# Kernel optimization log

Measured on AMD Instinct MI355X. Metric: run time of the kernel, lower is better.

Reference implementation:

```python
import jax, jax.numpy as jnp
import numpy as np

N = 100000       # nodes
E = 50000        # hyperedges
NNZ = 1600000    # incidence pairs
D = 128          # in_channels == heads*out_channels (heads=1)


def setup_inputs() -> dict:
    key = jax.random.key(0)
    k1, k2, k3, k4 = jax.random.split(key, 4)
    X = jax.random.normal(k1, (N, D), dtype=jnp.float32)
    W = jax.random.normal(k2, (D, D), dtype=jnp.float32) * (1.0 / np.sqrt(D))
    eps = jnp.zeros((1,), dtype=jnp.float32)
    vertex = jax.random.randint(k3, (NNZ,), 0, N, dtype=jnp.int32)
    edges = jax.random.randint(k4, (NNZ,), 0, E, dtype=jnp.int32)
    return {"X": X, "W": W, "eps": eps, "vertex": vertex, "edges": edges}


def reference(X, W, eps, vertex, edges):
    # X' = X W  (nn.Linear with no bias)
    Xp = X @ W                                    # [N, D]
    # vertex -> edge gather then scatter-mean (args.first_aggregate='mean')
    Xve = Xp[vertex]                              # [NNZ, D]
    Xe_sum = jax.ops.segment_sum(Xve, edges, num_segments=E)          # [E, D]
    cnt = jax.ops.segment_sum(jnp.ones((Xve.shape[0],), Xve.dtype), edges,
                              num_segments=E)                          # [E]
    Xe = Xe_sum / jnp.maximum(cnt, 1.0)[:, None]  # mean, empty edges -> 0
    # edge -> vertex gather then scatter-sum
    Xev = Xe[edges]                               # [NNZ, D]
    Xv = jax.ops.segment_sum(Xev, vertex, num_segments=N)             # [N, D]
    # GIN residual
    out = (1.0 + eps[0]) * Xp + Xv
    # args.use_norm: row-wise L2 normalize
    nrm = jnp.sqrt(jnp.sum(out * out, axis=-1, keepdims=True))
    out = out / jnp.maximum(nrm, 1e-12)
    return (out, Xe)
```

## Files before the change

kernel.cpp:

```cpp
#include <hip/hip_runtime.h>
#include <hip/hip_bf16.h>

#define NN   100000
#define NE   50000
#define NNZP 1600000
#define DD   128

#define EBK  512
#define NBE  ((NE + EBK - 1) / EBK)
#define VBK  512
#define NBV  ((NN + VBK - 1) / VBK)
#define NBT  (NBE + NBV)
#define CH2  3200
#define NSB  500
#define NGB  ((NN / 16 + 7) / 8)

typedef __attribute__((ext_vector_type(8))) short bf16x8;
typedef __attribute__((ext_vector_type(4))) float f32x4;
typedef __attribute__((ext_vector_type(4))) unsigned int u32x4;

__device__ __forceinline__ ushort f2bf(float f) {
    __hip_bfloat16 h = __float2bfloat16(f);
    return *reinterpret_cast<ushort*>(&h);
}
__device__ __forceinline__ void accQ(u32x4 u, float* a) {
    a[0] += __uint_as_float(u.x << 16);
    a[1] += __uint_as_float(u.x & 0xffff0000u);
    a[2] += __uint_as_float(u.y << 16);
    a[3] += __uint_as_float(u.y & 0xffff0000u);
    a[4] += __uint_as_float(u.z << 16);
    a[5] += __uint_as_float(u.z & 0xffff0000u);
    a[6] += __uint_as_float(u.w << 16);
    a[7] += __uint_as_float(u.w & 0xffff0000u);
}
__device__ __forceinline__ u32x4 ldg_u4(const ushort* p) {
    return *reinterpret_cast<const u32x4*>(p);
}

__device__ __forceinline__ void scan_gcnt(const int* __restrict__ gCnt,
                                          int* sbase, int* wsum) {
    const int t = threadIdx.x;
    int c0 = (2 * t     < NBT) ? gCnt[2 * t]     : 0;
    int c1 = (2 * t + 1 < NBT) ? gCnt[2 * t + 1] : 0;
    int s = c0 + c1;
    int inc = s;
    #pragma unroll
    for (int d = 1; d < 64; d <<= 1) {
        int x = __shfl_up(inc, d, 64);
        if ((t & 63) >= d) inc += x;
    }
    if ((t & 63) == 63) wsum[t >> 6] = inc;
    __syncthreads();
    int wid = t >> 6, wbase = 0;
    #pragma unroll
    for (int w = 0; w < 3; ++w) if (w < wid) wbase += wsum[w];
    int excl = wbase + inc - s;
    if (2 * t     < NBT) sbase[2 * t]     = excl;
    if (2 * t + 1 < NBT) sbase[2 * t + 1] = excl + c0;
    __syncthreads();
}

__global__ __launch_bounds__(256) void scatter_count(const int* __restrict__ vertex,
                                                     const int* __restrict__ edges,
                                                     int* __restrict__ blkCnt,
                                                     const float* __restrict__ W,
                                                     ushort* __restrict__ Wt) {
    __shared__ int c[NBT];
    const int t = threadIdx.x;
    if (blockIdx.x >= NSB) {
        int i = (blockIdx.x - NSB) * 256 + t;
        if (i < DD * DD) { int k = i >> 7, n = i & 127; Wt[n * DD + k] = f2bf(W[i]); }
        return;
    }
    for (int i = t; i < NBT; i += 256) c[i] = 0;
    __syncthreads();
    const int base = blockIdx.x * CH2;
    for (int i = t; i < CH2 / 4; i += 256) {
        int4 e4 = *reinterpret_cast<const int4*>(edges + base + i * 4);
        int4 v4 = *reinterpret_cast<const int4*>(vertex + base + i * 4);
        atomicAdd(&c[e4.x >> 9], 1); atomicAdd(&c[e4.y >> 9], 1);
        atomicAdd(&c[e4.z >> 9], 1); atomicAdd(&c[e4.w >> 9], 1);
        atomicAdd(&c[NBE + (v4.x >> 9)], 1); atomicAdd(&c[NBE + (v4.y >> 9)], 1);
        atomicAdd(&c[NBE + (v4.z >> 9)], 1); atomicAdd(&c[NBE + (v4.w >> 9)], 1);
    }
    __syncthreads();
    for (int i = t; i < NBT; i += 256) blkCnt[i * NSB + blockIdx.x] = c[i];
}

__global__ __launch_bounds__(256) void blk_scan(int* __restrict__ blkCnt,
                                                int* __restrict__ gCnt,
                                                int* __restrict__ eoff,
                                                int* __restrict__ voff) {
    __shared__ int wsum[4];
    const int t = threadIdx.x;
    if (blockIdx.x == 0 && t == 0) { eoff[NE] = NNZP; voff[NN] = NNZP; }
    int* p = blkCnt + blockIdx.x * NSB;
    int c0 = (2 * t     < NSB) ? p[2 * t]     : 0;
    int c1 = (2 * t + 1 < NSB) ? p[2 * t + 1] : 0;
    int s = c0 + c1;
    int inc = s;
    #pragma unroll
    for (int d = 1; d < 64; d <<= 1) {
        int x = __shfl_up(inc, d, 64);
        if ((t & 63) >= d) inc += x;
    }
    if ((t & 63) == 63) wsum[t >> 6] = inc;
    __syncthreads();
    int wid = t >> 6, wbase = 0;
    #pragma unroll
    for (int w = 0; w < 3; ++w) if (w < wid) wbase += wsum[w];
    int excl = wbase + inc - s;
    if (2 * t     < NSB) p[2 * t]     = excl;
    if (2 * t + 1 < NSB) p[2 * t + 1] = excl + c0;
    if (t == 255) gCnt[blockIdx.x] = wbase + inc;
}

__global__ __launch_bounds__(256) void place_gemm(const int* __restrict__ vertex,
                                                  const int* __restrict__ edges,
                                                  const int* __restrict__ blkCnt,
                                                  const int* __restrict__ gCnt,
                                                  unsigned int* __restrict__ ebuckP,
                                                  unsigned int* __restrict__ vbuckP,
                                                  const float* __restrict__ X,
                                                  const ushort* __restrict__ Wt,
                                                  ushort* __restrict__ Xp16) {
    __shared__ char smem[DD * DD * 2];
    __shared__ int wsum[4];
    const int t = threadIdx.x;
    if (blockIdx.x < NGB) {
        char* WtL = smem;
        for (int c = t; c < 2048; c += 256) {
            int n = c >> 4, kc = c & 15;
            int dst = (n * 256 + kc * 16) ^ ((n & 7) << 4);
            *reinterpret_cast<int4*>(WtL + dst) = reinterpret_cast<const int4*>(Wt)[c];
        }
        __syncthreads();
        int wave = t >> 6;
        int lane = t & 63;
        int r = lane & 15, half = lane >> 4;
        #pragma unroll
        for (int rt = 0; rt < 2; ++rt) {
            int rowTile = blockIdx.x * 8 + wave * 2 + rt;
            if (rowTile >= NN / 16) break;
            const float* xrow = X + (size_t)(rowTile * 16 + r) * DD;
            f32x4 acc[8];
            #pragma unroll
            for (int nt = 0; nt < 8; ++nt) acc[nt] = (f32x4)(0.f);
            #pragma unroll
            for (int kk = 0; kk < DD; kk += 32) {
                int kbase = kk + half * 8;
                float4 xa = *reinterpret_cast<const float4*>(xrow + kbase);
                float4 xb = *reinterpret_cast<const float4*>(xrow + kbase + 4);
                bf16x8 a;
                a[0] = (short)f2bf(xa.x); a[1] = (short)f2bf(xa.y);
                a[2] = (short)f2bf(xa.z); a[3] = (short)f2bf(xa.w);
                a[4] = (short)f2bf(xb.x); a[5] = (short)f2bf(xb.y);
                a[6] = (short)f2bf(xb.z); a[7] = (short)f2bf(xb.w);
                #pragma unroll
                for (int nt = 0; nt < 8; ++nt) {
                    int n = nt * 16 + r;
                    int off = (n * 256 + kbase * 2) ^ ((n & 7) << 4);
                    bf16x8 b = *reinterpret_cast<const bf16x8*>(WtL + off);
                    acc[nt] = __builtin_amdgcn_mfma_f32_16x16x32_bf16(a, b, acc[nt], 0, 0, 0);
                }
            }
            int row0 = rowTile * 16 + half * 4;
            #pragma unroll
            for (int nt = 0; nt < 8; ++nt)
                #pragma unroll
                for (int q = 0; q < 4; ++q)
                    Xp16[(size_t)(row0 + q) * DD + nt * 16 + r] = f2bf(acc[nt][q]);
        }
    } else {
        const int pb = blockIdx.x - NGB;
        int* sbase = reinterpret_cast<int*>(smem);
        int* cur   = sbase + NBT;
        scan_gcnt(gCnt, sbase, wsum);
        for (int i = t; i < NBT; i += 256) {
            int rel = blkCnt[i * NSB + pb];
            int b = sbase[i] - ((i < NBE) ? 0 : NNZP);
            cur[i] = b + rel;
        }
        __syncthreads();
        const int base = pb * CH2;
        for (int i = t; i < CH2 / 2; i += 256) {
            int2 e2 = *reinterpret_cast<const int2*>(edges + base + i * 2);
            int2 v2 = *reinterpret_cast<const int2*>(vertex + base + i * 2);
            int pe0 = atomicAdd(&cur[e2.x >> 9], 1);
            ebuckP[pe0] = ((unsigned)(e2.x & 511) << 17) | (unsigned)v2.x;
            int pe1 = atomicAdd(&cur[e2.y >> 9], 1);
            ebuckP[pe1] = ((unsigned)(e2.y & 511) << 17) | (unsigned)v2.y;
            int pv0 = atomicAdd(&cur[NBE + (v2.x >> 9)], 1);
            vbuckP[pv0] = ((unsigned)(v2.x & 511) << 16) | (unsigned)e2.x;
            int pv1 = atomicAdd(&cur[NBE + (v2.y >> 9)], 1);
            vbuckP[pv1] = ((unsigned)(v2.y & 511) << 16) | (unsigned)e2.y;
        }
    }
}

__global__ __launch_bounds__(256) void place_buckets2(const unsigned int* __restrict__ ebuckP,
                                                      const unsigned int* __restrict__ vbuckP,
                                                      const int* __restrict__ gCnt,
                                                      int* __restrict__ eoff,
                                                      int* __restrict__ voff,
                                                      int* __restrict__ vlist,
                                                      int* __restrict__ elist) {
    __shared__ int sbase[NBT];
    __shared__ int cnt[EBK];
    __shared__ int wsum[4];
    const int t = threadIdx.x;
    scan_gcnt(gCnt, sbase, wsum);
    int b = blockIdx.x;
    const unsigned int* buck; int id0, nid, start, end; int* off; int* lst;
    int sh_amt; unsigned msk;
    if (b < NBE) {
        buck = ebuckP; id0 = b * EBK; nid = min(EBK, NE - id0);
        start = sbase[b]; end = start + gCnt[b]; off = eoff; lst = vlist;
        sh_amt = 17; msk = 0x1FFFFu;
    } else {
        buck = vbuckP; id0 = (b - NBE) * VBK; nid = min(VBK, NN - id0);
        start = sbase[b] - NNZP; end = start + gCnt[b]; off = voff; lst = elist;
        sh_amt = 16; msk = 0xFFFFu;
    }
    for (int i = t; i < nid; i += 256) cnt[i] = 0;
    __syncthreads();
    for (int i = start + t; i < end; i += 256)
        atomicAdd(&cnt[buck[i] >> sh_amt], 1);
    __syncthreads();
    int c0 = (2 * t     < nid) ? cnt[2 * t]     : 0;
    int c1 = (2 * t + 1 < nid) ? cnt[2 * t + 1] : 0;
    int s = c0 + c1;
    int inc = s;
    #pragma unroll
    for (int d = 1; d < 64; d <<= 1) {
        int x = __shfl_up(inc, d, 64);
        if ((t & 63) >= d) inc += x;
    }
    if ((t & 63) == 63) wsum[t >> 6] = inc;
    __syncthreads();
    int wid = t >> 6, wbase = 0;
    #pragma unroll
    for (int w = 0; w < 3; ++w) if (w < wid) wbase += wsum[w];
    int excl = start + wbase + (inc - s);
    if (2 * t     < nid) off[id0 + 2 * t]     = excl;
    if (2 * t + 1 < nid) off[id0 + 2 * t + 1] = excl + c0;
    __syncthreads();
    if (2 * t     < nid) cnt[2 * t]     = excl;
    if (2 * t + 1 < nid) cnt[2 * t + 1] = excl + c0;
    __syncthreads();
    for (int i = start + t; i < end; i += 256) {
        unsigned p = buck[i];
        lst[atomicAdd(&cnt[p >> sh_amt], 1)] = (int)(p & msk);
    }
}

__global__ __launch_bounds__(256) void edge_gather(const ushort* __restrict__ Xp16,
                                                   const int* __restrict__ eoff,
                                                   const int* __restrict__ vlist,
                                                   float* __restrict__ Xe,
                                                   ushort* __restrict__ Xe16) {
    int e = blockIdx.x * 16 + (threadIdx.x >> 4);
    if (e >= NE) return;
    int lane = threadIdx.x & 15;
    int start = eoff[e], end = eoff[e + 1];
    float a[8] = {0.f, 0.f, 0.f, 0.f, 0.f, 0.f, 0.f, 0.f};
    int j = start;
    for (; j + 3 < end; j += 4) {
        int v0 = vlist[j], v1 = vlist[j + 1], v2 = vlist[j + 2], v3 = vlist[j + 3];
        u32x4 u0 = ldg_u4(Xp16 + (size_t)v0 * DD + lane * 8);
        u32x4 u1 = ldg_u4(Xp16 + (size_t)v1 * DD + lane * 8);
        u32x4 u2 = ldg_u4(Xp16 + (size_t)v2 * DD + lane * 8);
        u32x4 u3 = ldg_u4(Xp16 + (size_t)v3 * DD + lane * 8);
        accQ(u0, a); accQ(u1, a); accQ(u2, a); accQ(u3, a);
    }
    for (; j < end; ++j) {
        u32x4 u = ldg_u4(Xp16 + (size_t)vlist[j] * DD + lane * 8);
        accQ(u, a);
    }
    float inv = 1.0f / fmaxf((float)(end - start), 1.0f);
    f32x4 o0, o1;
    #pragma unroll
    for (int i = 0; i < 4; ++i) { o0[i] = a[i] * inv; o1[i] = a[4 + i] * inv; }
    float* xe = Xe + (size_t)e * DD + lane * 8;
    __builtin_nontemporal_store(o0, reinterpret_cast<f32x4*>(xe));
    __builtin_nontemporal_store(o1, reinterpret_cast<f32x4*>(xe + 4));
    ushort h[8];
    #pragma unroll
    for (int i = 0; i < 4; ++i) { h[i] = f2bf(o0[i]); h[4 + i] = f2bf(o1[i]); }
    *reinterpret_cast<int4*>(Xe16 + (size_t)e * DD + lane * 8) =
        *reinterpret_cast<const int4*>(h);
}

__global__ __launch_bounds__(256) void vertex_gather_out(const ushort* __restrict__ Xp16,
                                                         const ushort* __restrict__ Xe16,
                                                         const int* __restrict__ voff,
                                                         const int* __restrict__ elist,
                                                         const float* __restrict__ eps,
                                                         float* __restrict__ Out) {
    int v = blockIdx.x * 16 + (threadIdx.x >> 4);
    if (v >= NN) return;
    int lane = threadIdx.x & 15;
    int start = voff[v], end = voff[v + 1];
    float a[8] = {0.f, 0.f, 0.f, 0.f, 0.f, 0.f, 0.f, 0.f};
    int j = start;
    for (; j + 3 < end; j += 4) {
        int e0 = elist[j], e1 = elist[j + 1], e2 = elist[j + 2], e3 = elist[j + 3];
        u32x4 u0 = ldg_u4(Xe16 + (size_t)e0 * DD + lane * 8);
        u32x4 u1 = ldg_u4(Xe16 + (size_t)e1 * DD + lane * 8);
        u32x4 u2 = ldg_u4(Xe16 + (size_t)e2 * DD + lane * 8);
        u32x4 u3 = ldg_u4(Xe16 + (size_t)e3 * DD + lane * 8);
        accQ(u0, a); accQ(u1, a); accQ(u2, a); accQ(u3, a);
    }
    for (; j < end; ++j) {
        u32x4 u = ldg_u4(Xe16 + (size_t)elist[j] * DD + lane * 8);
        accQ(u, a);
    }
    float g = 1.0f + eps[0];
    u32x4 xp = __builtin_nontemporal_load(
        reinterpret_cast<const u32x4*>(Xp16 + (size_t)v * DD + lane * 8));
    float o[8];
    o[0] = fmaf(g, __uint_as_float(xp.x << 16),         a[0]);
    o[1] = fmaf(g, __uint_as_float(xp.x & 0xffff0000u), a[1]);
    o[2] = fmaf(g, __uint_as_float(xp.y << 16),         a[2]);
    o[3] = fmaf(g, __uint_as_float(xp.y & 0xffff0000u), a[3]);
    o[4] = fmaf(g, __uint_as_float(xp.z << 16),         a[4]);
    o[5] = fmaf(g, __uint_as_float(xp.z & 0xffff0000u), a[5]);
    o[6] = fmaf(g, __uint_as_float(xp.w << 16),         a[6]);
    o[7] = fmaf(g, __uint_as_float(xp.w & 0xffff0000u), a[7]);
    float ss = 0.f;
    #pragma unroll
    for (int i = 0; i < 8; ++i) ss += o[i] * o[i];
    #pragma unroll
    for (int off = 1; off < 16; off <<= 1) ss += __shfl_xor(ss, off, 64);
    float inv = 1.0f / fmaxf(sqrtf(ss), 1e-12f);
    f32x4 s0, s1;
    #pragma unroll
    for (int i = 0; i < 4; ++i) { s0[i] = o[i] * inv; s1[i] = o[4 + i] * inv; }
    float* op = Out + (size_t)v * DD + lane * 8;
    __builtin_nontemporal_store(s0, reinterpret_cast<f32x4*>(op));
    __builtin_nontemporal_store(s1, reinterpret_cast<f32x4*>(op + 4));
}

extern "C" void kernel_launch(void* const* d_in, const int* in_sizes, int n_in,
                              void* d_out, int out_size, void* d_ws, size_t ws_size,
                              hipStream_t stream) {
    const float* X      = (const float*)d_in[0];
    const float* W      = (const float*)d_in[1];
    const float* eps    = (const float*)d_in[2];
    const int*   vertex = (const int*)d_in[3];
    const int*   edges  = (const int*)d_in[4];

    float* out = (float*)d_out;
    float* Xe  = out + (size_t)NN * DD;

    unsigned int* ebuckP = (unsigned int*)out;
    unsigned int* vbuckP = ebuckP + NNZP;

    ushort* Xp16 = (ushort*)d_ws;
    ushort* Xe16 = Xp16 + (size_t)NN * DD;
    ushort* Wt16 = Xe16 + (size_t)NE * DD;
    int*    eoff = (int*)(Wt16 + DD * DD);
    int*    voff = eoff + NE + 1;
    int*    vlist = voff + NN + 1;
    int*    elist = vlist + NNZP;
    int*    gCnt  = elist + NNZP;
    int*    blkCnt = gCnt + NBT;

    scatter_count<<<NSB + 64, 256, 0, stream>>>(vertex, edges, blkCnt, W, Wt16);
    blk_scan<<<NBT, 256, 0, stream>>>(blkCnt, gCnt, eoff, voff);
    place_gemm<<<NGB + NSB, 256, 0, stream>>>(vertex, edges, blkCnt, gCnt,
                                              ebuckP, vbuckP, X, Wt16, Xp16);
    place_buckets2<<<NBT, 256, 0, stream>>>(ebuckP, vbuckP, gCnt, eoff, voff, vlist, elist);
    edge_gather<<<NE / 16, 256, 0, stream>>>(Xp16, eoff, vlist, Xe, Xe16);
    vertex_gather_out<<<NN / 16, 256, 0, stream>>>(Xp16, Xe16, voff, elist, eps, out);
}
```

Measured before the change: 206.3 us.

## Split bucket placement and overlap vertex placement with edge gather

The combined edge/vertex bucket placement kernel is split in two. Edge-bucket placement runs alone first, and vertex-bucket placement is merged into the edge_gather launch as extra leading blocks, so the two independent pieces of work share one grid. This shortens the critical path of the launch sequence, at the cost of heavier shared memory use in the fused kernel, which may lower occupancy for the gather blocks.

```diff
diff --git a/kernel.cpp b/kernel.cpp
--- a/kernel.cpp
+++ b/kernel.cpp
@@ -58,6 +58,45 @@
     if (2 * t     < NBT) sbase[2 * t]     = excl;
     if (2 * t + 1 < NBT) sbase[2 * t + 1] = excl + c0;
     __syncthreads();
+}
+
+__device__ __forceinline__ void place_bucket_body(const unsigned int* __restrict__ buck,
+                                                  int id0, int nid, int start, int end,
+                                                  int sh_amt, unsigned msk,
+                                                  int* __restrict__ off,
+                                                  int* __restrict__ lst,
+                                                  int* cnt, int* wsum) {
+    const int t = threadIdx.x;
+    for (int i = t; i < nid; i += 256) cnt[i] = 0;
+    __syncthreads();
+    for (int i = start + t; i < end; i += 256)
+        atomicAdd(&cnt[buck[i] >> sh_amt], 1);
+    __syncthreads();
+    int c0 = (2 * t     < nid) ? cnt[2 * t]     : 0;
+    int c1 = (2 * t + 1 < nid) ? cnt[2 * t + 1] : 0;
+    int s = c0 + c1;
+    int inc = s;
+    #pragma unroll
+    for (int d = 1; d < 64; d <<= 1) {
+        int x = __shfl_up(inc, d, 64);
+        if ((t & 63) >= d) inc += x;
+    }
+    if ((t & 63) == 63) wsum[t >> 6] = inc;
+    __syncthreads();
+    int wid = t >> 6, wbase = 0;
+    #pragma unroll
+    for (int w = 0; w < 3; ++w) if (w < wid) wbase += wsum[w];
+    int excl = start + wbase + (inc - s);
+    if (2 * t     < nid) off[id0 + 2 * t]     = excl;
+    if (2 * t + 1 < nid) off[id0 + 2 * t + 1] = excl + c0;
+    __syncthreads();
+    if (2 * t     < nid) cnt[2 * t]     = excl;
+    if (2 * t + 1 < nid) cnt[2 * t + 1] = excl + c0;
+    __syncthreads();
+    for (int i = start + t; i < end; i += 256) {
+        unsigned p = buck[i];
+        lst[atomicAdd(&cnt[p >> sh_amt], 1)] = (int)(p & msk);
+    }
 }
 
 __global__ __launch_bounds__(256) void scatter_count(const int* __restrict__ vertex,
@@ -198,68 +237,41 @@
     }
 }
 
-__global__ __launch_bounds__(256) void place_buckets2(const unsigned int* __restrict__ ebuckP,
-                                                      const unsigned int* __restrict__ vbuckP,
-                                                      const int* __restrict__ gCnt,
-                                                      int* __restrict__ eoff,
-                                                      int* __restrict__ voff,
-                                                      int* __restrict__ vlist,
-                                                      int* __restrict__ elist) {
+__global__ __launch_bounds__(256) void place_buckets_e(const unsigned int* __restrict__ ebuckP,
+                                                       const int* __restrict__ gCnt,
+                                                       int* __restrict__ eoff,
+                                                       int* __restrict__ vlist) {
     __shared__ int sbase[NBT];
     __shared__ int cnt[EBK];
     __shared__ int wsum[4];
-    const int t = threadIdx.x;
     scan_gcnt(gCnt, sbase, wsum);
     int b = blockIdx.x;
-    const unsigned int* buck; int id0, nid, start, end; int* off; int* lst;
-    int sh_amt; unsigned msk;
-    if (b < NBE) {
-        buck = ebuckP; id0 = b * EBK; nid = min(EBK, NE - id0);
-        start = sbase[b]; end = start + gCnt[b]; off = eoff; lst = vlist;
-        sh_amt = 17; msk = 0x1FFFFu;
-    } else {
-        buck = vbuckP; id0 = (b - NBE) * VBK; nid = min(VBK, NN - id0);
-        start = sbase[b] - NNZP; end = start + gCnt[b]; off = voff; lst = elist;
-        sh_amt = 16; msk = 0xFFFFu;
-    }
-    for (int i = t; i < nid; i += 256) cnt[i] = 0;
-    __syncthreads();
-    for (int i = start + t; i < end; i += 256)
-        atomicAdd(&cnt[buck[i] >> sh_amt], 1);
-    __syncthreads();
-    int c0 = (2 * t     < nid) ? cnt[2 * t]     : 0;
-    int c1 = (2 * t + 1 < nid) ? cnt[2 * t + 1] : 0;
-    int s = c0 + c1;
-    int inc = s;
-    #pragma unroll
-    for (int d = 1; d < 64; d <<= 1) {
-        int x = __shfl_up(inc, d, 64);
-        if ((t & 63) >= d) inc += x;
-    }
-    if ((t & 63) == 63) wsum[t >> 6] = inc;
-    __syncthreads();
-    int wid = t >> 6, wbase = 0;
-    #pragma unroll
-    for (int w = 0; w < 3; ++w) if (w < wid) wbase += wsum[w];
-    int excl = start + wbase + (inc - s);
-    if (2 * t     < nid) off[id0 + 2 * t]     = excl;
-    if (2 * t + 1 < nid) off[id0 + 2 * t + 1] = excl + c0;
-    __syncthreads();
-    if (2 * t     < nid) cnt[2 * t]     = excl;
-    if (2 * t + 1 < nid) cnt[2 * t + 1] = excl + c0;
-    __syncthreads();
-    for (int i = start + t; i < end; i += 256) {
-        unsigned p = buck[i];
-        lst[atomicAdd(&cnt[p >> sh_amt], 1)] = (int)(p & msk);
-    }
-}
-
-__global__ __launch_bounds__(256) void edge_gather(const ushort* __restrict__ Xp16,
-                                                   const int* __restrict__ eoff,
-                                                   const int* __restrict__ vlist,
-                                                   float* __restrict__ Xe,
-                                                   ushort* __restrict__ Xe16) {
-    int e = blockIdx.x * 16 + (threadIdx.x >> 4);
+    int id0 = b * EBK, nid = min(EBK, NE - id0);
+    int start = sbase[b], end = start + gCnt[b];
+    place_bucket_body(ebuckP, id0, nid, start, end, 17, 0x1FFFFu, eoff, vlist, cnt, wsum);
+}
+
+__global__ __launch_bounds__(256) void edge_gather_pbv(const ushort* __restrict__ Xp16,
+                                                       const int* __restrict__ eoff,
+                                                       const int* __restrict__ vlist,
+                                                       float* __restrict__ Xe,
+                                                       ushort* __restrict__ Xe16,
+                                                       const unsigned int* __restrict__ vbuckP,
+                                                       const int* __restrict__ gCnt,
+                                                       int* __restrict__ voff,
+                                                       int* __restrict__ elist) {
+    __shared__ int sbase[NBT];
+    __shared__ int cnt[VBK];
+    __shared__ int wsum[4];
+    if (blockIdx.x < NBV) {
+        scan_gcnt(gCnt, sbase, wsum);
+        int b = blockIdx.x;
+        int id0 = b * VBK, nid = min(VBK, NN - id0);
+        int start = sbase[NBE + b] - NNZP, end = start + gCnt[NBE + b];
+        place_bucket_body(vbuckP, id0, nid, start, end, 16, 0xFFFFu, voff, elist, cnt, wsum);
+        return;
+    }
+    int e = (blockIdx.x - NBV) * 16 + (threadIdx.x >> 4);
     if (e >= NE) return;
     int lane = threadIdx.x & 15;
     int start = eoff[e], end = eoff[e + 1];
@@ -370,7 +382,8 @@
     blk_scan<<<NBT, 256, 0, stream>>>(blkCnt, gCnt, eoff, voff);
     place_gemm<<<NGB + NSB, 256, 0, stream>>>(vertex, edges, blkCnt, gCnt,
                                               ebuckP, vbuckP, X, Wt16, Xp16);
-    place_buckets2<<<NBT, 256, 0, stream>>>(ebuckP, vbuckP, gCnt, eoff, voff, vlist, elist);
-    edge_gather<<<NE / 16, 256, 0, stream>>>(Xp16, eoff, vlist, Xe, Xe16);
+    place_buckets_e<<<NBE, 256, 0, stream>>>(ebuckP, gCnt, eoff, vlist);
+    edge_gather_pbv<<<NBV + NE / 16, 256, 0, stream>>>(Xp16, eoff, vlist, Xe, Xe16,
+                                                       vbuckP, gCnt, voff, elist);
     vertex_gather_out<<<NN / 16, 256, 0, stream>>>(Xp16, Xe16, voff, elist, eps, out);
 }
```

Measured after the change: 215.8 us. 1.05x slower.
